# Optimization experiments

Hardware: AMD Instinct MI355X
Metric: run time of the kernel (lower is better)

## Reference

```python
import jax, jax.numpy as jnp
import numpy as np

KERNEL = 7  # median blur window size (odd)


def setup_inputs() -> dict:
    key = jax.random.key(0)
    # NCHW image batch, values in [0,1) like normalized images
    img = jax.random.uniform(key, (8, 3, 512, 512), dtype=jnp.float32)
    return {"img": img}


def _median_blur(img, k):
    # Matches kornia.filters.median_blur: zero padding ('same'), then median
    # over the k*k window. k*k is odd so the exact middle of the sorted
    # window equals torch.median's lower median.
    pad = k // 2
    b, c, h, w = img.shape
    x = jnp.pad(img, ((0, 0), (0, 0), (pad, pad), (pad, pad)))  # zero pad
    # unfold: [B, C, k*k, H, W] — same materialization as kornia's conv2d
    # with binary one-hot kernels. Loop is over the fixed k*k = 49 taps.
    patches = jnp.stack(
        [x[:, :, i:i + h, j:j + w] for i in range(k) for j in range(k)],
        axis=2,
    )
    mid = (k * k) // 2
    return jnp.sort(patches, axis=2)[:, :, mid]  # [B, C, H, W]


def reference(img):
    return _median_blur(img, KERNEL)
```

## Files before the change

kernel.cpp:

```cpp
#include <hip/hip_runtime.h>
#include <utility>

#define IMG_H 512
#define IMG_W 512

typedef _Float16 h2 __attribute__((ext_vector_type(2)));
typedef _Float16 h16 __attribute__((ext_vector_type(16)));

__device__ __forceinline__ h2 h2min(h2 a, h2 b) { return __builtin_elementwise_min(a, b); }
__device__ __forceinline__ h2 h2max(h2 a, h2 b) { return __builtin_elementwise_max(a, b); }

struct Op { int kind, a, b, c; };
constexpr int NSLOT = 512;
constexpr int MAXOPS = 4096;
struct Prog { Op ops[MAXOPS]; int n; int nphys; bool ok; };

constexpr int pow2ceil(int x) { int p = 1; while (p < x) p += p; return p; }

struct Run { int s[48]; int len; };

struct Builder {
    Op ops[MAXOPS] = {};
    int n = 0;
    int nv = 0;
    bool ok = true;

    constexpr void emit(int k, int a, int b, int c) {
        if (n < MAXOPS) ops[n++] = Op{k, a, b, c}; else ok = false;
    }
    constexpr int fresh() {
        if (nv < NSLOT) return nv++;
        ok = false; return 0;
    }
    constexpr Run load_col(int c) {
        Run r{}; r.len = 7;
        for (int i = 0; i < 7; ++i) { r.s[i] = fresh(); emit(2, r.s[i], c * 7 + i, 0); }
        for (int p = 1; p < 7; p += p)
            for (int k = p; k > 0; k /= 2)
                for (int j = k % p; j + k < 7; j += k + k)
                    for (int i = 0; i < k; ++i)
                        if (i + j + k < 7 && (i + j) / (p + p) == (i + j + k) / (p + p))
                            emit(0, r.s[i + j], r.s[i + j + k], 0);
        return r;
    }
    constexpr Run copy(const Run& a) {
        Run r{}; r.len = a.len;
        for (int i = 0; i < a.len; ++i) { r.s[i] = fresh(); emit(1, r.s[i], a.s[i], 0); }
        return r;
    }
    constexpr Run merge(const Run& A, const Run& B) {
        int P = pow2ceil(A.len > B.len ? A.len : B.len);
        if (A.len > P || B.len > P || 2 * P > 96) { ok = false; }
        int map[96] = {};
        for (int i = 0; i < 2 * P; ++i) map[i] = -1;
        for (int i = 0; i < A.len; ++i) map[i] = A.s[i];
        for (int i = 0; i < B.len; ++i) map[P + i] = B.s[i];
        for (int k = P; k > 0; k /= 2)
            for (int j = k % P; j + k < 2 * P; j += k + k)
                for (int i = 0; i < k; ++i) {
                    int x = i + j, y = i + j + k;
                    int a = map[x], b = map[y];
                    if (a >= 0 && b >= 0) emit(0, a, b, 0);
                    else if (a < 0 && b >= 0) { map[x] = b; map[y] = -1; }
                }
        Run r{}; r.len = A.len + B.len;
        for (int i = 0; i < r.len; ++i) { if (map[i] < 0) ok = false; r.s[i] = map[i]; }
        for (int i = r.len; i < 2 * P; ++i) if (map[i] >= 0) ok = false;
        return r;
    }
    constexpr void select49(const Run& A, const Run& B, int o) {
        if (A.len != 42 || B.len != 7) ok = false;
        int T[7] = {};
        for (int t = 0; t < 7; ++t) {
            T[t] = fresh();
            emit(7, A.s[17 + t], B.s[6 - t], T[t]);
        }
        emit(4, T[0], T[1], 0); emit(4, T[2], T[3], 0);
        emit(4, T[4], T[5], 0); emit(4, T[6], A.s[24], 0);
        emit(4, T[0], T[2], 0); emit(4, T[4], T[6], 0);
        emit(4, T[0], T[4], 0);
        emit(3, o, T[0], 0);
    }
};

constexpr Prog build() {
    Builder b{};
    Run g1 = b.load_col(1), g2 = b.load_col(2), g3 = b.load_col(3),
        g4 = b.load_col(4), g5 = b.load_col(5), g6 = b.load_col(6),
        g7 = b.load_col(7), g8 = b.load_col(8);
    Run g2c = b.copy(g2), g4c = b.copy(g4), g6c = b.copy(g6);

    Run M12 = b.merge(g1, g2c);
    Run M34 = b.merge(g3, g4c);
    Run M56 = b.merge(g5, g6c);
    Run M56b = b.copy(M56);
    Run C28A = b.merge(M34, M56);
    Run C28Ac = b.copy(C28A);
    Run C42A = b.merge(C28Ac, M12);
    Run g0 = b.load_col(0);
    b.select49(C42A, g0, 0);
    b.select49(C42A, g7, 1);

    Run M78 = b.merge(g7, g8);
    Run M78b = b.copy(M78);
    Run C42B = b.merge(C28A, M78);
    Run g9 = b.load_col(9);
    b.select49(C42B, g2, 2);
    b.select49(C42B, g9, 3);

    Run g10 = b.load_col(10);
    Run M910 = b.merge(g9, g10);
    Run C28B = b.merge(M78b, M910);
    Run C28Bc = b.copy(C28B);
    Run C42C = b.merge(C28Bc, M56b);
    Run g11 = b.load_col(11);
    b.select49(C42C, g4, 4);
    b.select49(C42C, g11, 5);

    Run g12 = b.load_col(12);
    Run M1112 = b.merge(g11, g12);
    Run C42D = b.merge(C28B, M1112);
    Run g13 = b.load_col(13);
    b.select49(C42D, g6, 6);
    b.select49(C42D, g13, 7);

    Prog p{};
    bool needed[NSLOT] = {};
    int kindr[MAXOPS] = {};
    bool keep[MAXOPS] = {};
    for (int t = b.n - 1; t >= 0; --t) {
        Op o = b.ops[t];
        if (o.kind == 3) { keep[t] = true; kindr[t] = 3; needed[o.b] = true; }
        else if (o.kind == 0) {
            bool na = needed[o.a], nb = needed[o.b];
            if (na && nb)      { keep[t] = true; kindr[t] = 0; }
            else if (na)       { keep[t] = true; kindr[t] = 4; needed[o.b] = true; }
            else if (nb)       { keep[t] = true; kindr[t] = 5; needed[o.a] = true; }
        } else if (o.kind == 1) {
            if (needed[o.a]) { keep[t] = true; kindr[t] = 1; needed[o.a] = false; needed[o.b] = true; }
        } else if (o.kind == 2) {
            if (needed[o.a]) { keep[t] = true; kindr[t] = 2; needed[o.a] = false; }
        } else if (o.kind == 4) {
            if (needed[o.a]) { keep[t] = true; kindr[t] = 4; needed[o.b] = true; }
        } else if (o.kind == 5) {
            if (needed[o.b]) { keep[t] = true; kindr[t] = 5; needed[o.a] = true; }
        } else if (o.kind == 7) {
            if (needed[o.c]) { keep[t] = true; kindr[t] = 7; needed[o.c] = false;
                               needed[o.a] = true; needed[o.b] = true; }
        }
    }
    p.n = 0;
    for (int t = 0; t < b.n; ++t)
        if (keep[t]) { p.ops[p.n] = b.ops[t]; p.ops[p.n].kind = kindr[t]; ++p.n; }
    p.ok = b.ok;

    bool live[NSLOT] = {};
    bool lu_a[MAXOPS] = {};
    bool lu_b[MAXOPS] = {};
    for (int t = p.n - 1; t >= 0; --t) {
        Op o = p.ops[t];
        if (o.kind == 0 || o.kind == 4 || o.kind == 5 || o.kind == 7) {
            lu_a[t] = !live[o.a]; lu_b[t] = !live[o.b];
        } else if (o.kind == 1 || o.kind == 3) {
            lu_b[t] = !live[o.b];
        }
        if (o.kind == 0) { live[o.a] = false; live[o.b] = false; }
        else if (o.kind == 1 || o.kind == 2 || o.kind == 4) live[o.a] = false;
        else if (o.kind == 5) live[o.b] = false;
        else if (o.kind == 7) live[o.c] = false;
        if (o.kind == 0 || o.kind == 4 || o.kind == 5 || o.kind == 7) {
            live[o.a] = true; live[o.b] = true;
        } else if (o.kind == 1 || o.kind == 3) live[o.b] = true;
    }
    for (int t = 0; t < p.n; ++t) {
        Op o = p.ops[t];
        if (o.kind == 0 && (lu_a[t] || lu_b[t])) p.ok = false;
        if (o.kind == 4 && lu_a[t]) p.ok = false;
        if (o.kind == 5 && lu_b[t]) p.ok = false;
    }
    int phys[NSLOT] = {};
    bool bound[NSLOT] = {};
    int freelist[NSLOT] = {};
    int nfree = 0, nphys = 0;
    for (int t = 0; t < p.n; ++t) {
        Op o = p.ops[t];
        if (o.kind == 0) {
            if (!bound[o.a] || !bound[o.b]) p.ok = false;
            p.ops[t].a = phys[o.a]; p.ops[t].b = phys[o.b];
        } else if (o.kind == 4) {
            if (!bound[o.a] || !bound[o.b]) p.ok = false;
            p.ops[t].a = phys[o.a]; p.ops[t].b = phys[o.b];
            if (lu_b[t]) { freelist[nfree++] = phys[o.b]; bound[o.b] = false; }
        } else if (o.kind == 5) {
            if (!bound[o.a] || !bound[o.b]) p.ok = false;
            p.ops[t].a = phys[o.a]; p.ops[t].b = phys[o.b];
            if (lu_a[t]) { freelist[nfree++] = phys[o.a]; bound[o.a] = false; }
        } else if (o.kind == 7) {
            if (!bound[o.a] || !bound[o.b]) p.ok = false;
            p.ops[t].a = phys[o.a]; p.ops[t].b = phys[o.b];
            if (lu_a[t]) { freelist[nfree++] = phys[o.a]; bound[o.a] = false; }
            if (lu_b[t]) { freelist[nfree++] = phys[o.b]; bound[o.b] = false; }
            int pc = (nfree > 0) ? freelist[--nfree] : nphys++;
            phys[o.c] = pc; bound[o.c] = true;
            p.ops[t].c = pc;
        } else if (o.kind == 1) {
            if (!bound[o.b]) p.ok = false;
            int pb = phys[o.b];
            p.ops[t].b = pb;
            if (lu_b[t]) { freelist[nfree++] = pb; bound[o.b] = false; }
            int pa = (nfree > 0) ? freelist[--nfree] : nphys++;
            phys[o.a] = pa; bound[o.a] = true;
            p.ops[t].a = pa;
        } else if (o.kind == 2) {
            int pa = (nfree > 0) ? freelist[--nfree] : nphys++;
            phys[o.a] = pa; bound[o.a] = true;
            p.ops[t].a = pa;
        } else {
            if (!bound[o.b]) p.ok = false;
            p.ops[t].b = phys[o.b];
            if (lu_b[t]) { freelist[nfree++] = phys[o.b]; bound[o.b] = false; }
        }
        if (nphys > NSLOT || nfree > NSLOT) p.ok = false;
    }
    p.nphys = nphys;
    return p;
}

constexpr Prog PROG = build();
static_assert(PROG.ok, "program build failed");
static_assert(PROG.n > 300 && PROG.n < 2400, "op count out of range");
static_assert(PROG.nphys > 0 && PROG.nphys <= 256, "regalloc blew up");

template <int P>
__device__ __forceinline__ h2& vslot(h2* v0, h2* v1, h2* v2, h2* v3) {
    if constexpr (P < 64) return v0[P];
    else if constexpr (P < 128) return v1[P - 64];
    else if constexpr (P < 192) return v2[P - 128];
    else return v3[P - 192];
}
template <int P>
__device__ __forceinline__ h2 cslot(const h2* c0, const h2* c1) {
    if constexpr (P < 49) return c0[P];
    else return c1[P - 49];
}

template <int I>
__device__ __forceinline__ void step(h2* v0, h2* v1, h2* v2, h2* v3,
                                     const h2* c0, const h2* c1, h2* med) {
    constexpr Op o = PROG.ops[I];
    if constexpr (o.kind == 0) {
        h2& A = vslot<o.a>(v0, v1, v2, v3);
        h2& B = vslot<o.b>(v0, v1, v2, v3);
        h2 lo = h2min(A, B);
        h2 hi = h2max(A, B);
        A = lo; B = hi;
    } else if constexpr (o.kind == 1) {
        vslot<o.a>(v0, v1, v2, v3) = vslot<o.b>(v0, v1, v2, v3);
    } else if constexpr (o.kind == 2) {
        vslot<o.a>(v0, v1, v2, v3) = cslot<o.b>(c0, c1);
    } else if constexpr (o.kind == 3) {
        med[o.a] = vslot<o.b>(v0, v1, v2, v3);
    } else if constexpr (o.kind == 4) {
        h2& A = vslot<o.a>(v0, v1, v2, v3);
        A = h2min(A, vslot<o.b>(v0, v1, v2, v3));
    } else if constexpr (o.kind == 5) {
        h2& B = vslot<o.b>(v0, v1, v2, v3);
        B = h2max(vslot<o.a>(v0, v1, v2, v3), B);
    } else {
        vslot<o.c>(v0, v1, v2, v3) =
            h2max(vslot<o.a>(v0, v1, v2, v3), vslot<o.b>(v0, v1, v2, v3));
    }
}

template <size_t... Is>
__device__ __forceinline__ void run_all(h2* v0, h2* v1, h2* v2, h2* v3,
                                        const h2* c0, const h2* c1, h2* med,
                                        std::index_sequence<Is...>) {
    (step<(int)Is>(v0, v1, v2, v3, c0, c1, med), ...);
}

#define TW 528

__global__ __launch_bounds__(256, 2) void median7x7_kernel(
        const float* __restrict__ img, float* __restrict__ out) {
    const int bc = blockIdx.z;
    const int tx = threadIdx.x;
    const int ty = threadIdx.y;
    const int tid = ty * 64 + tx;
    const int yb = blockIdx.y * 8;
    const int x0 = tx * 8;

    const float* base = img + (size_t)bc * (IMG_H * IMG_W);

    __shared__ __align__(16) _Float16 tile[14][TW];

    const int col2 = tid * 2;
#pragma unroll
    for (int r = 0; r < 14; ++r) {
        const int gr = yb - 3 + r;
        float f0 = 0.f, f1 = 0.f;
        if ((unsigned)gr < IMG_H) {
            float2 q = *(const float2*)(base + (size_t)gr * IMG_W + col2);
            f0 = q.x; f1 = q.y;
        }
        *(h2*)&tile[r][4 + col2] = (h2)__builtin_amdgcn_cvt_pkrtz(f0, f1);
        if (tid < 8) {
            const int hi = (tid < 2) ? 2 * tid : 512 + 2 * tid;
            h2 z; z.x = (_Float16)0.f; z.y = (_Float16)0.f;
            *(h2*)&tile[r][hi] = z;
        }
    }
    __syncthreads();

    const int lbase = ty * 2;
    h16 row[8];
#pragma unroll
    for (int k = 0; k < 8; ++k)
        row[k] = *(const h16*)&tile[lbase + k][8 * tx];

    h2 c0[49], c1[49];
#pragma unroll
    for (int c = 0; c < 14; ++c) {
#pragma unroll
        for (int d = 0; d < 7; ++d) {
            h2 val;
            val.x = row[d][c + 1];
            val.y = row[d + 1][c + 1];
            const int idx = c * 7 + d;
            if (idx < 49) c0[idx] = val; else c1[idx - 49] = val;
        }
    }

    h2 va[64], vb[64], vc[64], vd[64];
    h2 med[8];
    run_all(va, vb, vc, vd, c0, c1, med, std::make_index_sequence<(size_t)PROG.n>{});

    const int y = yb + ty * 2;
    float* op = out + (size_t)bc * (IMG_H * IMG_W) + (size_t)y * IMG_W + x0;
    *(float4*)op = make_float4((float)med[0].x, (float)med[1].x,
                               (float)med[2].x, (float)med[3].x);
    *(float4*)(op + 4) = make_float4((float)med[4].x, (float)med[5].x,
                                     (float)med[6].x, (float)med[7].x);
    *(float4*)(op + IMG_W) = make_float4((float)med[0].y, (float)med[1].y,
                                         (float)med[2].y, (float)med[3].y);
    *(float4*)(op + IMG_W + 4) = make_float4((float)med[4].y, (float)med[5].y,
                                             (float)med[6].y, (float)med[7].y);
}

extern "C" void kernel_launch(void* const* d_in, const int* in_sizes, int n_in,
                              void* d_out, int out_size, void* d_ws, size_t ws_size,
                              hipStream_t stream) {
    const float* img = (const float*)d_in[0];
    float* out = (float*)d_out;
    dim3 grid(1, 64, 24);
    dim3 block(64, 4, 1);
    hipLaunchKernelGGL(median7x7_kernel, grid, block, 0, stream, img, out);
}
```

Measured before the change: 96.28 us.

## Store pre-paired half2 row pairs in padded LDS and load taps on demand

Changes the shared-memory tile so each entry already holds the packed pair of vertically adjacent pixels, with one padding slot every eight columns to avoid bank conflicts. The sorting network now reads each input tap straight from LDS when the program first needs it, instead of loading 8 h16 rows and building 98 packed tap registers up front. The aim is to cut register pressure (the register-allocation bound is tightened) and drop the shuffle and packing work. The cost is more individual LDS reads spread through the network, plus a more involved indexing scheme for the padding and the zero borders.

```diff
diff --git a/kernel.cpp b/kernel.cpp
--- a/kernel.cpp
+++ b/kernel.cpp
@@ -5,7 +5,6 @@
 #define IMG_W 512
 
 typedef _Float16 h2 __attribute__((ext_vector_type(2)));
-typedef _Float16 h16 __attribute__((ext_vector_type(16)));
 
 __device__ __forceinline__ h2 h2min(h2 a, h2 b) { return __builtin_elementwise_min(a, b); }
 __device__ __forceinline__ h2 h2max(h2 a, h2 b) { return __builtin_elementwise_max(a, b); }
@@ -229,7 +228,7 @@
 constexpr Prog PROG = build();
 static_assert(PROG.ok, "program build failed");
 static_assert(PROG.n > 300 && PROG.n < 2400, "op count out of range");
-static_assert(PROG.nphys > 0 && PROG.nphys <= 256, "regalloc blew up");
+static_assert(PROG.nphys > 0 && PROG.nphys <= 224, "regalloc blew up");
 
 template <int P>
 __device__ __forceinline__ h2& vslot(h2* v0, h2* v1, h2* v2, h2* v3) {
@@ -238,15 +237,12 @@
     else if constexpr (P < 192) return v2[P - 128];
     else return v3[P - 192];
 }
-template <int P>
-__device__ __forceinline__ h2 cslot(const h2* c0, const h2* c1) {
-    if constexpr (P < 49) return c0[P];
-    else return c1[P - 49];
-}
+
+#define LROW 594
 
 template <int I>
 __device__ __forceinline__ void step(h2* v0, h2* v1, h2* v2, h2* v3,
-                                     const h2* c0, const h2* c1, h2* med) {
+                                     const h2* __restrict__ ldsg, h2* med) {
     constexpr Op o = PROG.ops[I];
     if constexpr (o.kind == 0) {
         h2& A = vslot<o.a>(v0, v1, v2, v3);
@@ -257,7 +253,9 @@
     } else if constexpr (o.kind == 1) {
         vslot<o.a>(v0, v1, v2, v3) = vslot<o.b>(v0, v1, v2, v3);
     } else if constexpr (o.kind == 2) {
-        vslot<o.a>(v0, v1, v2, v3) = cslot<o.b>(c0, c1);
+        constexpr int cc = o.b / 7, ii = o.b % 7;
+        constexpr int off = ii * LROW + cc + (cc >= 8 ? 1 : 0);
+        vslot<o.a>(v0, v1, v2, v3) = ldsg[off];
     } else if constexpr (o.kind == 3) {
         med[o.a] = vslot<o.b>(v0, v1, v2, v3);
     } else if constexpr (o.kind == 4) {
@@ -274,12 +272,10 @@
 
 template <size_t... Is>
 __device__ __forceinline__ void run_all(h2* v0, h2* v1, h2* v2, h2* v3,
-                                        const h2* c0, const h2* c1, h2* med,
+                                        const h2* __restrict__ ldsg, h2* med,
                                         std::index_sequence<Is...>) {
-    (step<(int)Is>(v0, v1, v2, v3, c0, c1, med), ...);
-}
-
-#define TW 528
+    (step<(int)Is>(v0, v1, v2, v3, ldsg, med), ...);
+}
 
 __global__ __launch_bounds__(256, 2) void median7x7_kernel(
         const float* __restrict__ img, float* __restrict__ out) {
@@ -292,48 +288,42 @@
 
     const float* base = img + (size_t)bc * (IMG_H * IMG_W);
 
-    __shared__ __align__(16) _Float16 tile[14][TW];
-
-    const int col2 = tid * 2;
+    __shared__ h2 lds[13 * LROW];
+
+    const int cA = 2 * tid;
+    h2 pk[14];
 #pragma unroll
     for (int r = 0; r < 14; ++r) {
         const int gr = yb - 3 + r;
         float f0 = 0.f, f1 = 0.f;
         if ((unsigned)gr < IMG_H) {
-            float2 q = *(const float2*)(base + (size_t)gr * IMG_W + col2);
+            float2 q = *(const float2*)(base + (size_t)gr * IMG_W + cA);
             f0 = q.x; f1 = q.y;
         }
-        *(h2*)&tile[r][4 + col2] = (h2)__builtin_amdgcn_cvt_pkrtz(f0, f1);
-        if (tid < 8) {
-            const int hi = (tid < 2) ? 2 * tid : 512 + 2 * tid;
-            h2 z; z.x = (_Float16)0.f; z.y = (_Float16)0.f;
-            *(h2*)&tile[r][hi] = z;
-        }
+        pk[r] = (h2)__builtin_amdgcn_cvt_pkrtz(f0, f1);
+    }
+    const int LA = cA + 3, LB = cA + 4;
+    const int pA = LA + (LA >> 3), pB = LB + (LB >> 3);
+#pragma unroll
+    for (int p = 0; p < 13; ++p) {
+        h2 va; va.x = pk[p].x; va.y = pk[p + 1].x;
+        h2 vb; vb.x = pk[p].y; vb.y = pk[p + 1].y;
+        lds[p * LROW + pA] = va;
+        lds[p * LROW + pB] = vb;
+    }
+    if (tid < 78) {
+        const int row = tid / 6, w = tid % 6;
+        const int ph = (w < 3) ? w : (579 + (w - 3));
+        h2 z; z.x = (_Float16)0.f; z.y = (_Float16)0.f;
+        lds[row * LROW + ph] = z;
     }
     __syncthreads();
 
-    const int lbase = ty * 2;
-    h16 row[8];
-#pragma unroll
-    for (int k = 0; k < 8; ++k)
-        row[k] = *(const h16*)&tile[lbase + k][8 * tx];
-
-    h2 c0[49], c1[49];
-#pragma unroll
-    for (int c = 0; c < 14; ++c) {
-#pragma unroll
-        for (int d = 0; d < 7; ++d) {
-            h2 val;
-            val.x = row[d][c + 1];
-            val.y = row[d + 1][c + 1];
-            const int idx = c * 7 + d;
-            if (idx < 49) c0[idx] = val; else c1[idx - 49] = val;
-        }
-    }
+    const h2* ldsg = &lds[(2 * ty) * LROW + 9 * tx];
 
     h2 va[64], vb[64], vc[64], vd[64];
     h2 med[8];
-    run_all(va, vb, vc, vd, c0, c1, med, std::make_index_sequence<(size_t)PROG.n>{});
+    run_all(va, vb, vc, vd, ldsg, med, std::make_index_sequence<(size_t)PROG.n>{});
 
     const int y = yb + ty * 2;
     float* op = out + (size_t)bc * (IMG_H * IMG_W) + (size_t)y * IMG_W + x0;
```

Measured after the change: 89.70 us. 1.07x faster.
